# Kernel optimization log

Hardware: AMD Instinct MI355X
Metric: run time of the kernel (lower is better)

The kernel has to match this reference:

```python
import jax, jax.numpy as jnp
import numpy as np

EPS = 1e-7  # keras.backend.epsilon()
ROUTING_ITERS = 3


def squash(x, axis=-1):
    # squash(v) = (|v|^2 / (1+|v|^2)) * v/|v|
    sq = jnp.sum(jnp.square(x), axis=axis, keepdims=True)
    safe = jnp.sqrt(sq + EPS)
    return (sq / (1.0 + sq)) * (x / safe)


def setup_inputs() -> dict:
    key = jax.random.key(0)
    k1, k2 = jax.random.split(key)
    B, N_in, D_in = 32, 2048, 16
    N_out, D_out = 64, 32
    x = jax.random.normal(k1, (B, N_in, D_in), dtype=jnp.float32)
    # glorot-ish scale for transformation matrices
    W = jax.random.normal(k2, (N_in, N_out, D_out, D_in), dtype=jnp.float32) * 0.05
    bias = jnp.zeros((N_out, D_out), dtype=jnp.float32)
    return {"x": x, "W": W, "bias": bias}


def reference(x, W, bias):
    B = x.shape[0]
    N_in, N_out, D_out, D_in = W.shape
    # predictions u_hat[b,i,j,d] = sum_p W[i,j,d,p] * x[b,i,p]
    u_hat = jnp.einsum('bip,ijdp->bijd', x, W)  # (B, N_in, N_out, D_out)
    b_log = jnp.zeros((B, N_in, N_out), dtype=x.dtype)
    v = None
    for it in range(ROUTING_ITERS):
        c = jax.nn.softmax(b_log, axis=-1)                  # (B, N_in, N_out)
        s = jnp.einsum('bij,bijd->bjd', c, u_hat) + bias    # (B, N_out, D_out)
        v = squash(s, axis=-1)                              # (B, N_out, D_out)
        if it < ROUTING_ITERS - 1:
            b_log = b_log + jnp.einsum('bijd,bjd->bij', u_hat, v)
    return v
```

## Files before the change

### kernel.cpp

```cpp
#include <hip/hip_runtime.h>


#define B_   32
#define NI   2048
#define NO   64
#define DO_  32
#define DI   16
#define IC   64
#define NCHUNK (NI / IC)
#define NWAVE (NO * NCHUNK)

typedef __bf16 bf16x8 __attribute__((ext_vector_type(8)));
typedef float  f32x16 __attribute__((ext_vector_type(16)));

__global__ __launch_bounds__(256) void s_mfma_kernel(const float* __restrict__ W,
                                                     const float* __restrict__ x,
                                                     const float* __restrict__ c,
                                                     float* __restrict__ s)
{
    const int tid  = threadIdx.x;
    const int lane = tid & 63;
    const int wid  = blockIdx.x * 4 + (tid >> 6);
    const int j    = wid & 63;
    const int i0   = (wid >> 6) * IC;
    const int m    = lane & 31;
    const int h    = lane >> 5;

    const float* Wp = W + (((size_t)i0 * NO + j) * DO_ + m) * DI + 8 * h;
    const float* xp = x + ((size_t)m * NI + i0) * DI + 8 * h;
    const bool hasC = (c != nullptr);
    const float cunif = 1.0f / 64.0f;

    f32x16 acc;
    #pragma unroll
    for (int r = 0; r < 16; ++r) acc[r] = 0.0f;

    #pragma unroll 4
    for (int ii = 0; ii < IC; ++ii) {
        const float4 w0 = ((const float4*)Wp)[0];
        const float4 w1 = ((const float4*)Wp)[1];
        const float4 x0 = ((const float4*)xp)[0];
        const float4 x1 = ((const float4*)xp)[1];
        float cv = cunif;
        if (hasC) cv = c[(size_t)(i0 + ii) * (NO * B_) + j * B_ + m];

        bf16x8 af, bv;
        af[0] = (__bf16)w0.x; af[1] = (__bf16)w0.y; af[2] = (__bf16)w0.z; af[3] = (__bf16)w0.w;
        af[4] = (__bf16)w1.x; af[5] = (__bf16)w1.y; af[6] = (__bf16)w1.z; af[7] = (__bf16)w1.w;
        bv[0] = (__bf16)(cv * x0.x); bv[1] = (__bf16)(cv * x0.y);
        bv[2] = (__bf16)(cv * x0.z); bv[3] = (__bf16)(cv * x0.w);
        bv[4] = (__bf16)(cv * x1.x); bv[5] = (__bf16)(cv * x1.y);
        bv[6] = (__bf16)(cv * x1.z); bv[7] = (__bf16)(cv * x1.w);

        acc = __builtin_amdgcn_mfma_f32_32x32x16_bf16(af, bv, acc, 0, 0, 0);

        Wp += (size_t)NO * DO_ * DI;
        xp += DI;
    }

    #pragma unroll
    for (int r = 0; r < 16; ++r) {
        const int row = (r & 3) + 8 * (r >> 2) + 4 * h;
        atomicAdd(&s[((size_t)j * DO_ + row) * B_ + m], acc[r]);
    }
}

__global__ __launch_bounds__(256) void t_mfma_kernel(const float* __restrict__ W,
                                                     const float* __restrict__ x,
                                                     const float* __restrict__ vT,
                                                     float* __restrict__ t)
{
    const int tid  = threadIdx.x;
    const int lane = tid & 63;
    const int wid  = blockIdx.x * 4 + (tid >> 6);
    const int j    = wid & 63;
    const int i0   = (wid >> 6) * IC;
    const int m    = lane & 31;
    const int h    = lane >> 5;

    const float* Wp = W + (((size_t)i0 * NO + j) * DO_ + m) * DI + 8 * h;
    const float* xp = x + ((size_t)m * NI + i0) * DI + 8 * h;

    float vr[16];
    #pragma unroll
    for (int r = 0; r < 16; ++r) {
        const int row = (r & 3) + 8 * (r >> 2) + 4 * h;
        vr[r] = vT[((size_t)j * DO_ + row) * B_ + m];
    }

    #pragma unroll 2
    for (int ii = 0; ii < IC; ++ii) {
        const float4 w0 = ((const float4*)Wp)[0];
        const float4 w1 = ((const float4*)Wp)[1];
        const float4 x0 = ((const float4*)xp)[0];
        const float4 x1 = ((const float4*)xp)[1];

        bf16x8 af, bv;
        af[0] = (__bf16)w0.x; af[1] = (__bf16)w0.y; af[2] = (__bf16)w0.z; af[3] = (__bf16)w0.w;
        af[4] = (__bf16)w1.x; af[5] = (__bf16)w1.y; af[6] = (__bf16)w1.z; af[7] = (__bf16)w1.w;
        bv[0] = (__bf16)x0.x; bv[1] = (__bf16)x0.y; bv[2] = (__bf16)x0.z; bv[3] = (__bf16)x0.w;
        bv[4] = (__bf16)x1.x; bv[5] = (__bf16)x1.y; bv[6] = (__bf16)x1.z; bv[7] = (__bf16)x1.w;

        f32x16 z;
        #pragma unroll
        for (int r = 0; r < 16; ++r) z[r] = 0.0f;
        f32x16 u = __builtin_amdgcn_mfma_f32_32x32x16_bf16(af, bv, z, 0, 0, 0);

        float p0 = 0.f, p1 = 0.f, p2 = 0.f, p3 = 0.f;
        #pragma unroll
        for (int r = 0; r < 16; r += 4) {
            p0 = fmaf(u[r + 0], vr[r + 0], p0);
            p1 = fmaf(u[r + 1], vr[r + 1], p1);
            p2 = fmaf(u[r + 2], vr[r + 2], p2);
            p3 = fmaf(u[r + 3], vr[r + 3], p3);
        }
        float tp = (p0 + p1) + (p2 + p3);
        tp += __shfl_xor(tp, 32);
        if (h == 0) t[(size_t)(i0 + ii) * (NO * B_) + j * B_ + m] = tp;

        Wp += (size_t)NO * DO_ * DI;
        xp += DI;
    }
}

__global__ __launch_bounds__(256) void softmax_kernel(float* __restrict__ t)
{
    __shared__ float red[8][32];
    __shared__ float row_m[32];
    __shared__ float row_s[32];
    const int i = blockIdx.x;
    const int tid = threadIdx.x;
    const int b = tid & 31;
    const int g = tid >> 5;
    float* base = t + (size_t)i * (NO * B_);

    float tv[8];
    #pragma unroll
    for (int k = 0; k < 8; ++k) tv[k] = base[(g * 8 + k) * B_ + b];

    float m8 = tv[0];
    #pragma unroll
    for (int k = 1; k < 8; ++k) m8 = fmaxf(m8, tv[k]);
    red[g][b] = m8;
    __syncthreads();
    if (tid < 32) {
        float mm = red[0][tid];
        #pragma unroll
        for (int gg = 1; gg < 8; ++gg) mm = fmaxf(mm, red[gg][tid]);
        row_m[tid] = mm;
    }
    __syncthreads();
    const float mm = row_m[b];
    float e[8]; float ps = 0.f;
    #pragma unroll
    for (int k = 0; k < 8; ++k) { e[k] = __expf(tv[k] - mm); ps += e[k]; }
    __syncthreads();
    red[g][b] = ps;
    __syncthreads();
    if (tid < 32) {
        float ss = 0.f;
        #pragma unroll
        for (int gg = 0; gg < 8; ++gg) ss += red[gg][tid];
        row_s[tid] = 1.0f / ss;
    }
    __syncthreads();
    const float inv = row_s[b];
    #pragma unroll
    for (int k = 0; k < 8; ++k) base[(g * 8 + k) * B_ + b] = e[k] * inv;
}

__global__ __launch_bounds__(256) void squash_kernel(const float* __restrict__ s,
                                                     const float* __restrict__ bias,
                                                     const float* __restrict__ v0T,
                                                     float* __restrict__ out,
                                                     int mode)
{
    __shared__ float red[8][32];
    __shared__ float scl[32];
    const int j = blockIdx.x;
    const int tid = threadIdx.x;
    const int b = tid & 31;
    const int g = tid >> 5;
    const int d0 = g * 4;

    float sv[4];
    #pragma unroll
    for (int q = 0; q < 4; ++q)
        sv[q] = s[((size_t)j * DO_ + d0 + q) * B_ + b] + bias[j * DO_ + d0 + q];

    float p = 0.f;
    #pragma unroll
    for (int q = 0; q < 4; ++q) p = fmaf(sv[q], sv[q], p);
    red[g][b] = p;
    __syncthreads();
    if (tid < 32) {
        float n2 = 0.f;
        #pragma unroll
        for (int gg = 0; gg < 8; ++gg) n2 += red[gg][tid];
        scl[tid] = n2 / ((1.0f + n2) * sqrtf(n2 + 1e-7f));
    }
    __syncthreads();
    const float sc = scl[b];
    #pragma unroll
    for (int q = 0; q < 4; ++q) {
        const int d = d0 + q;
        const float vq = sv[q] * sc;
        if (mode == 0)      out[((size_t)j * DO_ + d) * B_ + b] = vq;
        else if (mode == 1) out[((size_t)j * DO_ + d) * B_ + b] =
                                v0T[((size_t)j * DO_ + d) * B_ + b] + vq;
        else                out[((size_t)b * NO + j) * DO_ + d] = vq;
    }
}

extern "C" void kernel_launch(void* const* d_in, const int* in_sizes, int n_in,
                              void* d_out, int out_size, void* d_ws, size_t ws_size,
                              hipStream_t stream)
{
    const float* x    = (const float*)d_in[0];
    const float* W    = (const float*)d_in[1];
    const float* bias = (const float*)d_in[2];
    float* out = (float*)d_out;

    float* t_buf = (float*)d_ws;
    float* s_buf = t_buf + (size_t)NI * NO * B_;
    float* v0T   = s_buf + (size_t)NO * DO_ * B_;
    float* vsT   = v0T  + (size_t)NO * DO_ * B_;

    const dim3 gW(NWAVE / 4), tW(256);
    const dim3 gSm(NI), gSq(NO);
    const size_t sBytes = (size_t)NO * DO_ * B_ * sizeof(float);

    hipMemsetAsync(s_buf, 0, sBytes, stream);
    s_mfma_kernel<<<gW, tW, 0, stream>>>(W, x, nullptr, s_buf);
    squash_kernel<<<gSq, tW, 0, stream>>>(s_buf, bias, nullptr, v0T, 0);

    t_mfma_kernel<<<gW, tW, 0, stream>>>(W, x, v0T, t_buf);
    softmax_kernel<<<gSm, tW, 0, stream>>>(t_buf);
    hipMemsetAsync(s_buf, 0, sBytes, stream);
    s_mfma_kernel<<<gW, tW, 0, stream>>>(W, x, t_buf, s_buf);
    squash_kernel<<<gSq, tW, 0, stream>>>(s_buf, bias, v0T, vsT, 1);

    t_mfma_kernel<<<gW, tW, 0, stream>>>(W, x, vsT, t_buf);
    softmax_kernel<<<gSm, tW, 0, stream>>>(t_buf);
    hipMemsetAsync(s_buf, 0, sBytes, stream);
    s_mfma_kernel<<<gW, tW, 0, stream>>>(W, x, t_buf, s_buf);
    squash_kernel<<<gSq, tW, 0, stream>>>(s_buf, bias, nullptr, out, 2);
}
```

Before: 633.9 us.

## Cache W and x in bf16 workspace, replace atomics with partial-sum reduction

The first pass reads fp32 W once and writes a bf16 copy to workspace, and x is pre-converted to bf16. Later s/t passes stream the half-size bf16 W, which cuts DRAM traffic on the 134MB weight tensor. The atomicAdd accumulation of s is replaced by per-chunk partial sums reduced through LDS and then summed in the squash kernel, which also removes the memsets. The s kernel now runs a separate MFMA per input capsule and scales by c in fp32, adding MFMA and VALU work and a 128MB workspace write in exchange for less bandwidth.

```diff
diff --git a/kernel.cpp b/kernel.cpp
--- a/kernel.cpp
+++ b/kernel.cpp
@@ -6,30 +6,38 @@
 #define NO   64
 #define DO_  32
 #define DI   16
-#define IC   64
-#define NCHUNK (NI / IC)
-#define NWAVE (NO * NCHUNK)
+#define IC   16
+#define WSTRIDE ((size_t)NO * DO_ * DI)
 
 typedef __bf16 bf16x8 __attribute__((ext_vector_type(8)));
 typedef float  f32x16 __attribute__((ext_vector_type(16)));
-
-__global__ __launch_bounds__(256) void s_mfma_kernel(const float* __restrict__ W,
-                                                     const float* __restrict__ x,
-                                                     const float* __restrict__ c,
-                                                     float* __restrict__ s)
-{
-    const int tid  = threadIdx.x;
-    const int lane = tid & 63;
-    const int wid  = blockIdx.x * 4 + (tid >> 6);
-    const int j    = wid & 63;
-    const int i0   = (wid >> 6) * IC;
-    const int m    = lane & 31;
-    const int h    = lane >> 5;
-
-    const float* Wp = W + (((size_t)i0 * NO + j) * DO_ + m) * DI + 8 * h;
-    const float* xp = x + ((size_t)m * NI + i0) * DI + 8 * h;
-    const bool hasC = (c != nullptr);
-    const float cunif = 1.0f / 64.0f;
+union U16B { uint4 u; bf16x8 v; };
+
+__global__ __launch_bounds__(256) void convert_x_kernel(const float* __restrict__ x,
+                                                        __bf16* __restrict__ xb)
+{
+    const int idx = (blockIdx.x * 256 + threadIdx.x) * 4;
+    const float4 f = *(const float4*)(x + idx);
+    __bf16 o[4] = {(__bf16)f.x, (__bf16)f.y, (__bf16)f.z, (__bf16)f.w};
+    *(uint2*)(xb + idx) = *(uint2*)o;
+}
+
+__global__ __launch_bounds__(256) void passA_kernel(const float* __restrict__ W,
+                                                    const __bf16* __restrict__ xb,
+                                                    __bf16* __restrict__ Wb,
+                                                    float* __restrict__ part)
+{
+    __shared__ float lds[4][1024];
+    const int tid = threadIdx.x, lane = tid & 63, w = tid >> 6;
+    const int j  = blockIdx.x & 63;
+    const int ch = blockIdx.x >> 6;
+    const int i0 = ch * 64 + w * IC;
+    const int m  = lane & 31, h = lane >> 5;
+
+    const size_t toff = (((size_t)i0 * NO + j) * DO_ + m) * DI + 8 * h;
+    const float*  Wp  = W  + toff;
+    __bf16*       Wbp = Wb + toff;
+    const __bf16* xp  = xb + ((size_t)m * NI + i0) * DI + 8 * h;
 
     f32x16 acc;
     #pragma unroll
@@ -39,47 +47,90 @@
     for (int ii = 0; ii < IC; ++ii) {
         const float4 w0 = ((const float4*)Wp)[0];
         const float4 w1 = ((const float4*)Wp)[1];
-        const float4 x0 = ((const float4*)xp)[0];
-        const float4 x1 = ((const float4*)xp)[1];
-        float cv = cunif;
-        if (hasC) cv = c[(size_t)(i0 + ii) * (NO * B_) + j * B_ + m];
-
-        bf16x8 af, bv;
-        af[0] = (__bf16)w0.x; af[1] = (__bf16)w0.y; af[2] = (__bf16)w0.z; af[3] = (__bf16)w0.w;
-        af[4] = (__bf16)w1.x; af[5] = (__bf16)w1.y; af[6] = (__bf16)w1.z; af[7] = (__bf16)w1.w;
-        bv[0] = (__bf16)(cv * x0.x); bv[1] = (__bf16)(cv * x0.y);
-        bv[2] = (__bf16)(cv * x0.z); bv[3] = (__bf16)(cv * x0.w);
-        bv[4] = (__bf16)(cv * x1.x); bv[5] = (__bf16)(cv * x1.y);
-        bv[6] = (__bf16)(cv * x1.z); bv[7] = (__bf16)(cv * x1.w);
-
-        acc = __builtin_amdgcn_mfma_f32_32x32x16_bf16(af, bv, acc, 0, 0, 0);
-
-        Wp += (size_t)NO * DO_ * DI;
-        xp += DI;
+        U16B a;
+        a.v[0] = (__bf16)w0.x; a.v[1] = (__bf16)w0.y; a.v[2] = (__bf16)w0.z; a.v[3] = (__bf16)w0.w;
+        a.v[4] = (__bf16)w1.x; a.v[5] = (__bf16)w1.y; a.v[6] = (__bf16)w1.z; a.v[7] = (__bf16)w1.w;
+        *(uint4*)Wbp = a.u;
+        U16B b; b.u = *(const uint4*)xp;
+        acc = __builtin_amdgcn_mfma_f32_32x32x16_bf16(a.v, b.v, acc, 0, 0, 0);
+        Wp += WSTRIDE; Wbp += WSTRIDE; xp += DI;
     }
 
     #pragma unroll
     for (int r = 0; r < 16; ++r) {
         const int row = (r & 3) + 8 * (r >> 2) + 4 * h;
-        atomicAdd(&s[((size_t)j * DO_ + row) * B_ + m], acc[r]);
-    }
-}
-
-__global__ __launch_bounds__(256) void t_mfma_kernel(const float* __restrict__ W,
-                                                     const float* __restrict__ x,
-                                                     const float* __restrict__ vT,
-                                                     float* __restrict__ t)
-{
-    const int tid  = threadIdx.x;
-    const int lane = tid & 63;
-    const int wid  = blockIdx.x * 4 + (tid >> 6);
-    const int j    = wid & 63;
-    const int i0   = (wid >> 6) * IC;
-    const int m    = lane & 31;
-    const int h    = lane >> 5;
-
-    const float* Wp = W + (((size_t)i0 * NO + j) * DO_ + m) * DI + 8 * h;
-    const float* xp = x + ((size_t)m * NI + i0) * DI + 8 * h;
+        lds[w][row * 32 + m] = acc[r];
+    }
+    __syncthreads();
+    float* pb = part + ((size_t)ch * NO + j) * 1024;
+    #pragma unroll
+    for (int q = 0; q < 4; ++q) {
+        const int idx = tid + 256 * q;
+        pb[idx] = lds[0][idx] + lds[1][idx] + lds[2][idx] + lds[3][idx];
+    }
+}
+
+__global__ __launch_bounds__(256) void s_kernel(const __bf16* __restrict__ Wb,
+                                                const __bf16* __restrict__ xb,
+                                                const float* __restrict__ c,
+                                                float* __restrict__ part)
+{
+    __shared__ float lds[4][1024];
+    const int tid = threadIdx.x, lane = tid & 63, w = tid >> 6;
+    const int j  = blockIdx.x & 63;
+    const int ch = blockIdx.x >> 6;
+    const int i0 = ch * 64 + w * IC;
+    const int m  = lane & 31, h = lane >> 5;
+
+    const __bf16* Wp = Wb + (((size_t)i0 * NO + j) * DO_ + m) * DI + 8 * h;
+    const __bf16* xp = xb + ((size_t)m * NI + i0) * DI + 8 * h;
+    const float*  cp = c  + (size_t)i0 * (NO * B_) + j * B_ + m;
+
+    f32x16 acc;
+    #pragma unroll
+    for (int r = 0; r < 16; ++r) acc[r] = 0.0f;
+
+    #pragma unroll 4
+    for (int ii = 0; ii < IC; ++ii) {
+        U16B a; a.u = *(const uint4*)Wp;
+        U16B b; b.u = *(const uint4*)xp;
+        const float cv = *cp;
+        f32x16 z;
+        #pragma unroll
+        for (int r = 0; r < 16; ++r) z[r] = 0.0f;
+        f32x16 u = __builtin_amdgcn_mfma_f32_32x32x16_bf16(a.v, b.v, z, 0, 0, 0);
+        #pragma unroll
+        for (int r = 0; r < 16; ++r) acc[r] = fmaf(cv, u[r], acc[r]);
+        Wp += WSTRIDE; xp += DI; cp += NO * B_;
+    }
+
+    #pragma unroll
+    for (int r = 0; r < 16; ++r) {
+        const int row = (r & 3) + 8 * (r >> 2) + 4 * h;
+        lds[w][row * 32 + m] = acc[r];
+    }
+    __syncthreads();
+    float* pb = part + ((size_t)ch * NO + j) * 1024;
+    #pragma unroll
+    for (int q = 0; q < 4; ++q) {
+        const int idx = tid + 256 * q;
+        pb[idx] = lds[0][idx] + lds[1][idx] + lds[2][idx] + lds[3][idx];
+    }
+}
+
+__global__ __launch_bounds__(256) void t_kernel(const __bf16* __restrict__ Wb,
+                                                const __bf16* __restrict__ xb,
+                                                const float* __restrict__ vT,
+                                                float* __restrict__ t)
+{
+    const int tid = threadIdx.x, lane = tid & 63;
+    const int wid = blockIdx.x * 4 + (tid >> 6);
+    const int j   = wid & 63;
+    const int i0  = (wid >> 6) * IC;
+    const int m   = lane & 31, h = lane >> 5;
+
+    const __bf16* Wp = Wb + (((size_t)i0 * NO + j) * DO_ + m) * DI + 8 * h;
+    const __bf16* xp = xb + ((size_t)m * NI + i0) * DI + 8 * h;
 
     float vr[16];
     #pragma unroll
@@ -88,23 +139,14 @@
         vr[r] = vT[((size_t)j * DO_ + row) * B_ + m];
     }
 
-    #pragma unroll 2
+    #pragma unroll 4
     for (int ii = 0; ii < IC; ++ii) {
-        const float4 w0 = ((const float4*)Wp)[0];
-        const float4 w1 = ((const float4*)Wp)[1];
-        const float4 x0 = ((const float4*)xp)[0];
-        const float4 x1 = ((const float4*)xp)[1];
-
-        bf16x8 af, bv;
-        af[0] = (__bf16)w0.x; af[1] = (__bf16)w0.y; af[2] = (__bf16)w0.z; af[3] = (__bf16)w0.w;
-        af[4] = (__bf16)w1.x; af[5] = (__bf16)w1.y; af[6] = (__bf16)w1.z; af[7] = (__bf16)w1.w;
-        bv[0] = (__bf16)x0.x; bv[1] = (__bf16)x0.y; bv[2] = (__bf16)x0.z; bv[3] = (__bf16)x0.w;
-        bv[4] = (__bf16)x1.x; bv[5] = (__bf16)x1.y; bv[6] = (__bf16)x1.z; bv[7] = (__bf16)x1.w;
-
+        U16B a; a.u = *(const uint4*)Wp;
+        U16B b; b.u = *(const uint4*)xp;
         f32x16 z;
         #pragma unroll
         for (int r = 0; r < 16; ++r) z[r] = 0.0f;
-        f32x16 u = __builtin_amdgcn_mfma_f32_32x32x16_bf16(af, bv, z, 0, 0, 0);
+        f32x16 u = __builtin_amdgcn_mfma_f32_32x32x16_bf16(a.v, b.v, z, 0, 0, 0);
 
         float p0 = 0.f, p1 = 0.f, p2 = 0.f, p3 = 0.f;
         #pragma unroll
@@ -117,9 +159,7 @@
         float tp = (p0 + p1) + (p2 + p3);
         tp += __shfl_xor(tp, 32);
         if (h == 0) t[(size_t)(i0 + ii) * (NO * B_) + j * B_ + m] = tp;
-
-        Wp += (size_t)NO * DO_ * DI;
-        xp += DI;
+        Wp += WSTRIDE; xp += DI;
     }
 }
 
@@ -169,11 +209,11 @@
     for (int k = 0; k < 8; ++k) base[(g * 8 + k) * B_ + b] = e[k] * inv;
 }
 
-__global__ __launch_bounds__(256) void squash_kernel(const float* __restrict__ s,
+__global__ __launch_bounds__(256) void squash_kernel(const float* __restrict__ part,
                                                      const float* __restrict__ bias,
                                                      const float* __restrict__ v0T,
                                                      float* __restrict__ out,
-                                                     int mode)
+                                                     int mode, float prescale)
 {
     __shared__ float red[8][32];
     __shared__ float scl[32];
@@ -185,13 +225,18 @@
 
     float sv[4];
     #pragma unroll
-    for (int q = 0; q < 4; ++q)
-        sv[q] = s[((size_t)j * DO_ + d0 + q) * B_ + b] + bias[j * DO_ + d0 + q];
-
-    float p = 0.f;
-    #pragma unroll
-    for (int q = 0; q < 4; ++q) p = fmaf(sv[q], sv[q], p);
-    red[g][b] = p;
+    for (int q = 0; q < 4; ++q) {
+        const float* p = part + (size_t)j * 1024 + (d0 + q) * 32 + b;
+        float a = 0.f;
+        #pragma unroll
+        for (int ch = 0; ch < 32; ++ch) a += p[(size_t)ch * NO * 1024];
+        sv[q] = a * prescale + bias[j * DO_ + d0 + q];
+    }
+
+    float p2s = 0.f;
+    #pragma unroll
+    for (int q = 0; q < 4; ++q) p2s = fmaf(sv[q], sv[q], p2s);
+    red[g][b] = p2s;
     __syncthreads();
     if (tid < 32) {
         float n2 = 0.f;
@@ -221,28 +266,29 @@
     const float* bias = (const float*)d_in[2];
     float* out = (float*)d_out;
 
-    float* t_buf = (float*)d_ws;
-    float* s_buf = t_buf + (size_t)NI * NO * B_;
-    float* v0T   = s_buf + (size_t)NO * DO_ * B_;
-    float* vsT   = v0T  + (size_t)NO * DO_ * B_;
-
-    const dim3 gW(NWAVE / 4), tW(256);
-    const dim3 gSm(NI), gSq(NO);
-    const size_t sBytes = (size_t)NO * DO_ * B_ * sizeof(float);
-
-    hipMemsetAsync(s_buf, 0, sBytes, stream);
-    s_mfma_kernel<<<gW, tW, 0, stream>>>(W, x, nullptr, s_buf);
-    squash_kernel<<<gSq, tW, 0, stream>>>(s_buf, bias, nullptr, v0T, 0);
-
-    t_mfma_kernel<<<gW, tW, 0, stream>>>(W, x, v0T, t_buf);
+    char* ws = (char*)d_ws;
+    __bf16* Wb   = (__bf16*)ws;
+    __bf16* xb   = (__bf16*)(ws + (size_t)134217728);
+    float*  t_buf= (float*) (ws + (size_t)134217728 + 2097152);
+    float*  part = (float*) (ws + (size_t)134217728 + 2097152 + 16777216);
+    float*  v0T  = (float*) (ws + (size_t)134217728 + 2097152 + 16777216 + 8388608);
+    float*  vsT  = v0T + (size_t)NO * DO_ * B_;
+
+    const dim3 tW(256);
+    const dim3 gX(1024), gP(2048), gSm(NI), gSq(NO);
+
+    convert_x_kernel<<<gX, tW, 0, stream>>>(x, xb);
+
+    passA_kernel<<<gP, tW, 0, stream>>>(W, xb, Wb, part);
+    squash_kernel<<<gSq, tW, 0, stream>>>(part, bias, nullptr, v0T, 0, 1.0f / 64.0f);
+
+    t_kernel<<<gP, tW, 0, stream>>>(Wb, xb, v0T, t_buf);
     softmax_kernel<<<gSm, tW, 0, stream>>>(t_buf);
-    hipMemsetAsync(s_buf, 0, sBytes, stream);
-    s_mfma_kernel<<<gW, tW, 0, stream>>>(W, x, t_buf, s_buf);
-    squash_kernel<<<gSq, tW, 0, stream>>>(s_buf, bias, v0T, vsT, 1);
-
-    t_mfma_kernel<<<gW, tW, 0, stream>>>(W, x, vsT, t_buf);
+    s_kernel<<<gP, tW, 0, stream>>>(Wb, xb, t_buf, part);
+    squash_kernel<<<gSq, tW, 0, stream>>>(part, bias, v0T, vsT, 1, 1.0f);
+
+    t_kernel<<<gP, tW, 0, stream>>>(Wb, xb, vsT, t_buf);
     softmax_kernel<<<gSm, tW, 0, stream>>>(t_buf);
-    hipMemsetAsync(s_buf, 0, sBytes, stream);
-    s_mfma_kernel<<<gW, tW, 0, stream>>>(W, x, t_buf, s_buf);
-    squash_kernel<<<gSq, tW, 0, stream>>>(s_buf, bias, nullptr, out, 2);
-}
+    s_kernel<<<gP, tW, 0, stream>>>(Wb, xb, t_buf, part);
+    squash_kernel<<<gSq, tW, 0, stream>>>(part, bias, nullptr, out, 2, 1.0f);
+}
```

After: 543.2 us. -14.3%, faster.
